# Performance work log

Measured on AMD Instinct MI355X. Metric: run time of the kernel, lower is better.

The kernel has to match this reference:

```python
import jax, jax.numpy as jnp
import numpy as np

NUM_HEADS = 8
ROPE_BASE = 10000.0


def _rope_cache(T, D, dtype=jnp.float32):
    # LLaMA-style rope cache: cos/sin of shape [T, D]
    inv_freq = 1.0 / (ROPE_BASE ** (jnp.arange(0, D, 2, dtype=dtype) / D))
    t = jnp.arange(T, dtype=dtype)
    freqs = t[:, None] * inv_freq[None, :]            # [T, D/2]
    emb = jnp.concatenate([freqs, freqs], axis=-1)    # [T, D]
    return jnp.cos(emb), jnp.sin(emb)


def _rotate_half(x):
    x1, x2 = jnp.split(x, 2, axis=-1)
    return jnp.concatenate([-x2, x1], axis=-1)


def setup_inputs() -> dict:
    key = jax.random.key(0)
    k1, k2, k3 = jax.random.split(key, 3)
    B, T, C = 4, 2048, 512
    x = jax.random.normal(k1, (B, T, C), dtype=jnp.float32)
    Wqkv = jax.random.normal(k2, (C, 3 * C), dtype=jnp.float32) * (1.0 / np.sqrt(C))
    Wproj = jax.random.normal(k3, (C, C), dtype=jnp.float32) * (1.0 / np.sqrt(C))
    return {"x": x, "Wqkv": Wqkv, "Wproj": Wproj}


def reference(x, Wqkv, Wproj):
    B, T, C = x.shape
    H = NUM_HEADS
    D = C // H

    qkv = jnp.einsum('btc,cf->btf', x, Wqkv)          # [B,T,3C]
    qkv = qkv.reshape(B, T, H, 3 * D)
    q, k, v = jnp.split(qkv, 3, axis=-1)              # each [B,T,H,D]
    q = q.transpose(0, 2, 1, 3)                       # [B,H,T,D]
    k = k.transpose(0, 2, 1, 3)
    v = v.transpose(0, 2, 1, 3)

    cos, sin = _rope_cache(T, D, dtype=x.dtype)       # [T,D]
    cos = cos[None, None, :, :]
    sin = sin[None, None, :, :]
    q = q * cos + _rotate_half(q) * sin
    k = k * cos + _rotate_half(k) * sin

    scale = 1.0 / np.sqrt(D)
    scores = jnp.einsum('bhqd,bhkd->bhqk', q, k) * scale  # [B,H,T,T]
    causal = jnp.tril(jnp.ones((T, T), dtype=bool))
    scores = jnp.where(causal[None, None, :, :], scores, jnp.finfo(scores.dtype).min)
    attn = jax.nn.softmax(scores, axis=-1)
    out = jnp.einsum('bhqk,bhkd->bhqd', attn, v)      # [B,H,T,D]
    out = out.transpose(0, 2, 1, 3).reshape(B, T, C)
    return jnp.einsum('btc,cd->btd', out, Wproj)
```

## Files before the change

kernel.cpp:

```cpp
#include <hip/hip_runtime.h>
#include <hip/hip_bf16.h>
#include <stdint.h>

constexpr int Bn = 4;
constexpr int Tn = 2048;
constexpr int Cn = 512;
constexpr int Hn = 8;
constexpr int Dn = 64;
constexpr int BT = Bn * Tn;
constexpr int NQKV = 3 * Cn;

typedef __attribute__((ext_vector_type(4))) float  f32x4;
typedef __attribute__((ext_vector_type(8))) short  s16x8;
typedef __attribute__((ext_vector_type(4))) short  s16x4;

__device__ __forceinline__ short f2bs(float f) {
    __hip_bfloat16 h = __float2bfloat16(f);
    return *reinterpret_cast<short*>(&h);
}

__device__ __forceinline__ void gload16(const short* g, short* l) {
    __builtin_amdgcn_global_load_lds(
        (const __attribute__((address_space(1))) void*)g,
        (__attribute__((address_space(3))) void*)l, 16, 0, 0);
}

__device__ const uint32_t UT[48] = {
    (31u<<16)|(0u<<8)|16u, (31u<<16)|(16u<<8)|32u, (30u<<16)|(15u<<8)|31u, (15u<<16)|(0u<<8)|16u,
    (30u<<16)|(0u<<8)|15u, (29u<<16)|(0u<<8)|15u, (29u<<16)|(15u<<8)|30u, (28u<<16)|(14u<<8)|29u, (14u<<16)|(0u<<8)|15u,
    (28u<<16)|(0u<<8)|14u, (27u<<16)|(0u<<8)|14u, (27u<<16)|(14u<<8)|28u, (26u<<16)|(13u<<8)|27u, (13u<<16)|(0u<<8)|14u,
    (26u<<16)|(0u<<8)|13u, (25u<<16)|(0u<<8)|13u, (25u<<16)|(13u<<8)|26u, (24u<<16)|(12u<<8)|25u, (12u<<16)|(0u<<8)|13u,
    (24u<<16)|(0u<<8)|12u, (23u<<16)|(0u<<8)|12u, (23u<<16)|(12u<<8)|24u, (22u<<16)|(11u<<8)|23u, (11u<<16)|(0u<<8)|12u,
    (22u<<16)|(0u<<8)|11u, (21u<<16)|(0u<<8)|11u, (21u<<16)|(11u<<8)|22u, (20u<<16)|(10u<<8)|21u, (10u<<16)|(0u<<8)|11u,
    (20u<<16)|(0u<<8)|10u, (19u<<16)|(0u<<8)|10u, (19u<<16)|(10u<<8)|20u, (18u<<16)|(9u<<8)|19u,  (9u<<16)|(0u<<8)|10u,
    (18u<<16)|(0u<<8)|9u,  (17u<<16)|(0u<<8)|9u,  (17u<<16)|(9u<<8)|18u,  (16u<<16)|(8u<<8)|17u,  (8u<<16)|(0u<<8)|9u,
    (16u<<16)|(0u<<8)|8u,  (7u<<16)|(0u<<8)|8u,
    (6u<<16)|(0u<<8)|7u, (5u<<16)|(0u<<8)|6u, (4u<<16)|(0u<<8)|5u, (3u<<16)|(0u<<8)|4u,
    (2u<<16)|(0u<<8)|3u, (1u<<16)|(0u<<8)|2u, (0u<<16)|(0u<<8)|1u
};


__global__ __launch_bounds__(256) void k_conv_x(const float* __restrict__ x,
                                                short* __restrict__ xb) {
    int i = blockIdx.x * 256 + threadIdx.x;
    f32x4 v = reinterpret_cast<const f32x4*>(x)[i];
    s16x4 o;
    o[0] = f2bs(v[0]); o[1] = f2bs(v[1]); o[2] = f2bs(v[2]); o[3] = f2bs(v[3]);
    reinterpret_cast<s16x4*>(xb)[i] = o;
}

__global__ __launch_bounds__(256) void k_wTt(const float* __restrict__ Wqkv,
                                             const float* __restrict__ Wproj,
                                             short* __restrict__ wqkvT,
                                             short* __restrict__ wprojT) {
    int bid = blockIdx.x;
    const float* W; short* out; int N, n0, k0;
    if (bid < 192) {
        W = Wqkv; out = wqkvT; N = NQKV;
        n0 = (bid >> 3) * 64; k0 = (bid & 7) * 64;
    } else {
        bid -= 192;
        W = Wproj; out = wprojT; N = Cn;
        n0 = (bid >> 3) * 64; k0 = (bid & 7) * 64;
    }
    __shared__ float lds[64 * 65];
    const int tid = threadIdx.x;
#pragma unroll
    for (int i = 0; i < 16; ++i) {
        int flat = i * 256 + tid;
        int k = flat >> 6, n = flat & 63;
        lds[n * 65 + k] = W[(size_t)(k0 + k) * N + n0 + n];
    }
    __syncthreads();
#pragma unroll
    for (int i = 0; i < 16; ++i) {
        int flat = i * 256 + tid;
        int n = flat >> 6, k = flat & 63;
        out[(size_t)(n0 + n) * 512 + k0 + k] = f2bs(lds[n * 65 + k]);
    }
}

__global__ __launch_bounds__(256) void k_rope(float2* __restrict__ csT) {
    int i = blockIdx.x * 256 + threadIdx.x;
    int t = i >> 6, d = i & 63;
    float inv = exp2f(-(float)(d & 31) * 0.41524101186f);
    float fr = (float)t * inv;
    csT[i] = make_float2(cosf(fr), sinf(fr));
}


template <int MODE>
__global__ __launch_bounds__(256, 2) void gemm_kernel(
    const short* __restrict__ A, const short* __restrict__ Bt,
    const float2* __restrict__ csT,
    short* __restrict__ Qb, short* __restrict__ Kb, short* __restrict__ Vt,
    float* __restrict__ outF) {
    const int m0 = blockIdx.y * 128;
    const int n0 = blockIdx.x * 128;
    const int tid = threadIdx.x;
    const int w = tid >> 6, lane = tid & 63;
    const int qi = lane & 15, g = lane >> 4;
    const int wr = w >> 1, wc = w & 1;

    __shared__ short As[2][128 * 64];
    __shared__ short Bs[2][128 * 64];

    f32x4 acc[4][4];
#pragma unroll
    for (int mt = 0; mt < 4; ++mt)
#pragma unroll
        for (int nt = 0; nt < 4; ++nt) acc[mt][nt] = (f32x4){0.f, 0.f, 0.f, 0.f};

    const int lr = lane >> 3;
    const int lc = (lane & 7) ^ lr;

#define STAGEG(buf, k0)                                                         \
    {                                                                           \
        _Pragma("unroll")                                                       \
        for (int s4_ = 0; s4_ < 4; ++s4_) {                                     \
            int slot_ = s4_ * 4 + w;                                            \
            int r_ = slot_ * 8 + lr;                                            \
            gload16(&A[(size_t)(m0 + r_) * 512 + (k0) + lc * 8],                \
                    &As[buf][slot_ * 512 + lane * 8]);                          \
            gload16(&Bt[(size_t)(n0 + r_) * 512 + (k0) + lc * 8],               \
                    &Bs[buf][slot_ * 512 + lane * 8]);                          \
        }                                                                       \
    }

    STAGEG(0, 0);
    __syncthreads();

    for (int it = 0; it < 8; ++it) {
        if (it + 1 < 8) STAGEG((it + 1) & 1, (it + 1) * 64);
        const int cur = it & 1;
#pragma unroll
        for (int kk = 0; kk < 2; ++kk) {
            s16x8 af[4], bf[4];
#pragma unroll
            for (int mt = 0; mt < 4; ++mt) {
                int row = wr * 64 + mt * 16 + qi;
                af[mt] = *(const s16x8*)&As[cur][row * 64 + (((kk << 2) | g) ^ (qi & 7)) * 8];
            }
#pragma unroll
            for (int nt = 0; nt < 4; ++nt) {
                int row = wc * 64 + nt * 16 + qi;
                bf[nt] = *(const s16x8*)&Bs[cur][row * 64 + (((kk << 2) | g) ^ (qi & 7)) * 8];
            }
#pragma unroll
            for (int mt = 0; mt < 4; ++mt)
#pragma unroll
                for (int nt = 0; nt < 4; ++nt)
                    acc[mt][nt] = __builtin_amdgcn_mfma_f32_16x16x32_bf16(
                        af[mt], bf[nt], acc[mt][nt], 0, 0, 0);
        }
        __syncthreads();
    }
#undef STAGEG

    if (MODE == 1) {
#pragma unroll
        for (int mt = 0; mt < 4; ++mt)
#pragma unroll
            for (int nt = 0; nt < 4; ++nt)
#pragma unroll
                for (int r = 0; r < 4; ++r)
                    outF[(size_t)(m0 + wr * 64 + mt * 16 + 4 * g + r) * 512 +
                         n0 + wc * 64 + nt * 16 + qi] = acc[mt][nt][r];
    } else {
        const int seg64 = (n0 >> 6) + wc;
        const int h = seg64 / 3;
        const int seg = seg64 % 3;
        const int b = m0 >> 11;
        const int tb = (m0 & 2047) + wr * 64;
        const float QSC = 0.125f * 1.44269504f;
        if (seg == 2) {
            const size_t vbase = (size_t)(b * Hn + h) * Dn;
#pragma unroll
            for (int mt = 0; mt < 4; ++mt)
#pragma unroll
                for (int nt = 0; nt < 4; ++nt)
#pragma unroll
                    for (int r = 0; r < 4; ++r) {
                        int t = tb + mt * 16 + 4 * g + r;
                        int d = nt * 16 + qi;
                        int o = t & 31;
                        int jj = (t & ~31) + ((o >> 2) & 3) * 8 + (o >> 4) * 4 + (o & 3);
                        Vt[(vbase + d) * Tn + jj] = f2bs(acc[mt][nt][r]);
                    }
        } else {
            short* dst = (seg == 0) ? Qb : Kb;
            const float post = (seg == 0) ? QSC : 1.0f;
            const size_t headbase = (size_t)(b * Hn + h) * Tn;
#pragma unroll
            for (int mt = 0; mt < 4; ++mt)
#pragma unroll
                for (int nt = 0; nt < 4; ++nt)
#pragma unroll
                    for (int r = 0; r < 4; ++r) {
                        int t = tb + mt * 16 + 4 * g + r;
                        int d = nt * 16 + qi;
                        float val = acc[mt][nt][r];
                        float pv = (nt < 2) ? -acc[mt][nt + 2][r] : acc[mt][nt - 2][r];
                        float2 cs = csT[t * 64 + d];
                        dst[(headbase + t) * Dn + d] = f2bs((val * cs.x + pv * cs.y) * post);
                    }
        }
    }
}


__global__ __launch_bounds__(256, 4) void attn_kernel(const short* __restrict__ Qb,
                                                      const short* __restrict__ Kb,
                                                      const short* __restrict__ Vt,
                                                      short* __restrict__ AO,
                                                      float* __restrict__ Opart,
                                                      float* __restrict__ Lpart) {
    const int idx = blockIdx.x;
    const int bh = idx & 31;
    const uint32_t e = UT[idx >> 5];
    const int qt = e >> 16;
    const int chlo = (e >> 8) & 255, chhi = e & 255;
    const int q0 = qt * 64;
    const int tid = threadIdx.x;
    const int w = tid >> 6, lane = tid & 63;
    const int qi = lane & 15, g = lane >> 4;
    const int b = bh >> 3, h = bh & 7;

    __shared__ short Ks[2][64 * 64];
    __shared__ short Vs[2][64 * 64];

    const short* Qh = Qb + (size_t)bh * Tn * Dn;
    const short* Kh = Kb + (size_t)bh * Tn * Dn;
    const short* Vh = Vt + (size_t)bh * Dn * Tn;

    const int wrow0 = q0 + w * 16;
    s16x8 qf[2];
#pragma unroll
    for (int dh = 0; dh < 2; ++dh)
        qf[dh] = *(const s16x8*)&Qh[(size_t)(wrow0 + qi) * Dn + dh * 32 + g * 8];

    f32x4 O[4];
#pragma unroll
    for (int dt = 0; dt < 4; ++dt) O[dt] = (f32x4){0.f, 0.f, 0.f, 0.f};
    float lsum = 0.f;

    const f32x4 z4 = {0.f, 0.f, 0.f, 0.f};

    const int lr = lane >> 3;
    const int lc = (lane & 7) ^ lr;

#define STAGE(buf, ch)                                                          \
    {                                                                           \
        const int kv0_ = (ch) * 64;                                             \
        _Pragma("unroll")                                                       \
        for (int i_ = 0; i_ < 2; ++i_) {                                        \
            int slot_ = i_ * 4 + w;                                             \
            int r_ = slot_ * 8 + lr;                                            \
            gload16(&Kh[(size_t)(kv0_ + r_) * 64 + lc * 8],                     \
                    &Ks[buf][slot_ * 512 + lane * 8]);                          \
            gload16(&Vh[(size_t)r_ * Tn + kv0_ + lc * 8],                       \
                    &Vs[buf][slot_ * 512 + lane * 8]);                          \
        }                                                                       \
    }

    STAGE(0, chlo);
    __syncthreads();

    for (int ch = chlo; ch < chhi; ++ch) {
        const int rel = ch - chlo;
        if (ch + 1 < chhi) STAGE((rel + 1) & 1, ch + 1);
        const int kv0 = ch * 64;
        const int cur = rel & 1;

        if (kv0 <= wrow0 + 15) {
            f32x4 sacc[4];
#pragma unroll
            for (int sub = 0; sub < 4; ++sub) {
                const int krow = sub * 16 + qi;
                s16x8 ka = *(const s16x8*)&Ks[cur][krow * 64 + ((g ^ (qi & 7))) * 8];
                s16x8 kc = *(const s16x8*)&Ks[cur][krow * 64 + (((4 | g) ^ (qi & 7))) * 8];
                f32x4 t0 = __builtin_amdgcn_mfma_f32_16x16x32_bf16(ka, qf[0], z4, 0, 0, 0);
                sacc[sub] = __builtin_amdgcn_mfma_f32_16x16x32_bf16(kc, qf[1], t0, 0, 0, 0);
            }

            float pe[16];
            if (kv0 + 63 <= wrow0) {
#pragma unroll
                for (int e2 = 0; e2 < 16; ++e2)
                    pe[e2] = exp2f(sacc[e2 >> 2][e2 & 3]);
            } else {
                const int qrow = wrow0 + qi;
#pragma unroll
                for (int sub = 0; sub < 4; ++sub)
#pragma unroll
                    for (int r = 0; r < 4; ++r) {
                        int key = kv0 + sub * 16 + 4 * g + r;
                        pe[sub * 4 + r] = (key <= qrow) ? exp2f(sacc[sub][r]) : 0.f;
                    }
            }
            {
                float a0 = (pe[0] + pe[1]) + (pe[2] + pe[3]);
                float a1 = (pe[4] + pe[5]) + (pe[6] + pe[7]);
                float a2 = (pe[8] + pe[9]) + (pe[10] + pe[11]);
                float a3 = (pe[12] + pe[13]) + (pe[14] + pe[15]);
                lsum += (a0 + a1) + (a2 + a3);
            }
            s16x8 pf[2];
#pragma unroll
            for (int c = 0; c < 2; ++c)
#pragma unroll
                for (int e2 = 0; e2 < 8; ++e2) pf[c][e2] = f2bs(pe[c * 8 + e2]);

#pragma unroll
            for (int c = 0; c < 2; ++c)
#pragma unroll
                for (int dt = 0; dt < 4; ++dt) {
                    const int vrow = dt * 16 + qi;
                    s16x8 vf = *(const s16x8*)&Vs[cur][vrow * 64 +
                                                       ((((c << 2) | g) ^ (qi & 7))) * 8];
                    O[dt] = __builtin_amdgcn_mfma_f32_16x16x32_bf16(
                        pf[c], vf, O[dt], 0, 0, 0);
                }
        }
        __syncthreads();
    }
#undef STAGE

    lsum += __shfl_xor(lsum, 16);
    lsum += __shfl_xor(lsum, 32);

    if (qt < 16) {
#pragma unroll
        for (int r = 0; r < 4; ++r) {
            float li = __shfl(lsum, 4 * g + r);
            float inv = 1.f / li;
            int t = wrow0 + 4 * g + r;
#pragma unroll
            for (int dt = 0; dt < 4; ++dt)
                AO[((size_t)(b * Tn + t)) * Cn + h * 64 + dt * 16 + qi] =
                    f2bs(O[dt][r] * inv);
        }
    } else {
        const int pu = (bh * 16 + (qt - 16)) * 2 + (chlo ? 1 : 0);
        float* Op = Opart + (size_t)pu * 4096;
        if (g == 0) Lpart[pu * 64 + w * 16 + qi] = lsum;
#pragma unroll
        for (int r = 0; r < 4; ++r) {
            int lrow = w * 16 + 4 * g + r;
#pragma unroll
            for (int dt = 0; dt < 4; ++dt)
                Op[lrow * 64 + dt * 16 + qi] = O[dt][r];
        }
    }
}


__global__ __launch_bounds__(256) void combine_kernel(const float* __restrict__ Opart,
                                                      const float* __restrict__ Lpart,
                                                      short* __restrict__ AO) {
    const int u = blockIdx.x;
    const int bh = u & 31, sqt = u >> 5;
    const int pu = (bh * 16 + sqt) * 2;
    const int row = threadIdx.x >> 2;
    const int d0 = (threadIdx.x & 3) * 16;

    const float* O0 = Opart + (size_t)pu * 4096 + row * 64 + d0;
    const float* O1 = O0 + 4096;
    float l = Lpart[pu * 64 + row] + Lpart[(pu + 1) * 64 + row];
    float inv = 1.f / l;

    const int b = bh >> 3, h = bh & 7;
    const int t = (16 + sqt) * 64 + row;
    short* dst = &AO[((size_t)(b * Tn + t)) * Cn + h * 64 + d0];

    s16x8 ov;
#pragma unroll
    for (int j = 0; j < 8; ++j) ov[j] = f2bs((O0[j] + O1[j]) * inv);
    *(s16x8*)dst = ov;
#pragma unroll
    for (int j = 0; j < 8; ++j) ov[j] = f2bs((O0[8 + j] + O1[8 + j]) * inv);
    *(s16x8*)(dst + 8) = ov;
}


extern "C" void kernel_launch(void* const* d_in, const int* in_sizes, int n_in,
                              void* d_out, int out_size, void* d_ws, size_t ws_size,
                              hipStream_t stream) {
    const float* x = (const float*)d_in[0];
    const float* Wqkv = (const float*)d_in[1];
    const float* Wproj = (const float*)d_in[2];
    float* out = (float*)d_out;

    char* ws = (char*)d_ws;
    size_t o = 0;
    short* xb = (short*)(ws + o);      o += (size_t)BT * Cn * 2;
    short* wqkvT = (short*)(ws + o);   o += (size_t)NQKV * Cn * 2;
    short* wprojT = (short*)(ws + o);  o += (size_t)Cn * Cn * 2;
    short* Qb = (short*)(ws + o);      o += (size_t)Bn * Hn * Tn * Dn * 2;
    short* Kb = (short*)(ws + o);      o += (size_t)Bn * Hn * Tn * Dn * 2;
    short* Vt = (short*)(ws + o);      o += (size_t)Bn * Hn * Tn * Dn * 2;
    float2* csT = (float2*)(ws + o);   o += (size_t)Tn * Dn * 8;
    float* Opart = (float*)(ws + o);   o += (size_t)512 * 2 * 4096 * 4;
    float* Lpart = (float*)(ws + o);   o += (size_t)512 * 2 * 64 * 4;

    k_conv_x<<<BT * Cn / 4 / 256, 256, 0, stream>>>(x, xb);
    k_wTt<<<dim3(256), 256, 0, stream>>>(Wqkv, Wproj, wqkvT, wprojT);
    k_rope<<<Tn * Dn / 256, 256, 0, stream>>>(csT);

    gemm_kernel<0><<<dim3(NQKV / 128, BT / 128), 256, 0, stream>>>(
        xb, wqkvT, csT, Qb, Kb, Vt, nullptr);

    attn_kernel<<<dim3(48 * 32), 256, 0, stream>>>(Qb, Kb, Vt, xb ,
                                                   Opart, Lpart);

    combine_kernel<<<dim3(512), 256, 0, stream>>>(Opart, Lpart, xb );

    gemm_kernel<1><<<dim3(Cn / 128, BT / 128), 256, 0, stream>>>(
        xb , wprojT, csT, nullptr, nullptr, nullptr, out);
}
```

Measured before the change: 95.93 us.

## Merge prep kernels into one launch and fuse split-KV combine via atomic counter

The three preprocessing kernels (x conversion, weight transpose, rope cache) become one launch, with an extra block that zeroes a counter array. The separate combine kernel is removed. For split query tiles, each attention block writes its partial result, fences, and increments an atomic counter. The second block to finish reads the other partial and writes the normalized output. This removes two kernel launches and one pass over the partial buffers, at the cost of a threadfence, an atomic, and a divergent tail in the last attention blocks.

```diff
diff --git a/kernel.cpp b/kernel.cpp
--- a/kernel.cpp
+++ b/kernel.cpp
@@ -40,52 +40,58 @@
 };
 
 
-__global__ __launch_bounds__(256) void k_conv_x(const float* __restrict__ x,
-                                                short* __restrict__ xb) {
-    int i = blockIdx.x * 256 + threadIdx.x;
-    f32x4 v = reinterpret_cast<const f32x4*>(x)[i];
-    s16x4 o;
-    o[0] = f2bs(v[0]); o[1] = f2bs(v[1]); o[2] = f2bs(v[2]); o[3] = f2bs(v[3]);
-    reinterpret_cast<s16x4*>(xb)[i] = o;
-}
-
-__global__ __launch_bounds__(256) void k_wTt(const float* __restrict__ Wqkv,
-                                             const float* __restrict__ Wproj,
-                                             short* __restrict__ wqkvT,
-                                             short* __restrict__ wprojT) {
-    int bid = blockIdx.x;
-    const float* W; short* out; int N, n0, k0;
-    if (bid < 192) {
-        W = Wqkv; out = wqkvT; N = NQKV;
-        n0 = (bid >> 3) * 64; k0 = (bid & 7) * 64;
+__global__ __launch_bounds__(256) void k_prep(const float* __restrict__ x,
+                                              const float* __restrict__ Wqkv,
+                                              const float* __restrict__ Wproj,
+                                              short* __restrict__ xb,
+                                              short* __restrict__ wqkvT,
+                                              short* __restrict__ wprojT,
+                                              float2* __restrict__ csT,
+                                              int* __restrict__ cnt) {
+    const int bid = blockIdx.x;
+    const int tid = threadIdx.x;
+    __shared__ float lds[64 * 65];
+
+    if (bid < 4096) {
+        int i = bid * 256 + tid;
+        f32x4 v = reinterpret_cast<const f32x4*>(x)[i];
+        s16x4 o;
+        o[0] = f2bs(v[0]); o[1] = f2bs(v[1]); o[2] = f2bs(v[2]); o[3] = f2bs(v[3]);
+        reinterpret_cast<s16x4*>(xb)[i] = o;
+    } else if (bid < 4352) {
+        int wb = bid - 4096;
+        const float* W; short* out; int N, n0, k0;
+        if (wb < 192) {
+            W = Wqkv; out = wqkvT; N = NQKV;
+            n0 = (wb >> 3) * 64; k0 = (wb & 7) * 64;
+        } else {
+            wb -= 192;
+            W = Wproj; out = wprojT; N = Cn;
+            n0 = (wb >> 3) * 64; k0 = (wb & 7) * 64;
+        }
+#pragma unroll
+        for (int i = 0; i < 16; ++i) {
+            int flat = i * 256 + tid;
+            int k = flat >> 6, n = flat & 63;
+            lds[n * 65 + k] = W[(size_t)(k0 + k) * N + n0 + n];
+        }
+        __syncthreads();
+#pragma unroll
+        for (int i = 0; i < 16; ++i) {
+            int flat = i * 256 + tid;
+            int n = flat >> 6, k = flat & 63;
+            out[(size_t)(n0 + n) * 512 + k0 + k] = f2bs(lds[n * 65 + k]);
+        }
+    } else if (bid < 4864) {
+        int i = (bid - 4352) * 256 + tid;
+        int t = i >> 6, d = i & 63;
+        float inv = exp2f(-(float)(d & 31) * 0.41524101186f);
+        float fr = (float)t * inv;
+        csT[i] = make_float2(cosf(fr), sinf(fr));
     } else {
-        bid -= 192;
-        W = Wproj; out = wprojT; N = Cn;
-        n0 = (bid >> 3) * 64; k0 = (bid & 7) * 64;
-    }
-    __shared__ float lds[64 * 65];
-    const int tid = threadIdx.x;
-#pragma unroll
-    for (int i = 0; i < 16; ++i) {
-        int flat = i * 256 + tid;
-        int k = flat >> 6, n = flat & 63;
-        lds[n * 65 + k] = W[(size_t)(k0 + k) * N + n0 + n];
-    }
-    __syncthreads();
-#pragma unroll
-    for (int i = 0; i < 16; ++i) {
-        int flat = i * 256 + tid;
-        int n = flat >> 6, k = flat & 63;
-        out[(size_t)(n0 + n) * 512 + k0 + k] = f2bs(lds[n * 65 + k]);
-    }
-}
-
-__global__ __launch_bounds__(256) void k_rope(float2* __restrict__ csT) {
-    int i = blockIdx.x * 256 + threadIdx.x;
-    int t = i >> 6, d = i & 63;
-    float inv = exp2f(-(float)(d & 31) * 0.41524101186f);
-    float fr = (float)t * inv;
-    csT[i] = make_float2(cosf(fr), sinf(fr));
+        cnt[tid] = 0;
+        cnt[tid + 256] = 0;
+    }
 }
 
 
@@ -214,7 +220,8 @@
                                                       const short* __restrict__ Vt,
                                                       short* __restrict__ AO,
                                                       float* __restrict__ Opart,
-                                                      float* __restrict__ Lpart) {
+                                                      float* __restrict__ Lpart,
+                                                      int* __restrict__ cnt) {
     const int idx = blockIdx.x;
     const int bh = idx & 31;
     const uint32_t e = UT[idx >> 5];
@@ -228,6 +235,7 @@
 
     __shared__ short Ks[2][64 * 64];
     __shared__ short Vs[2][64 * 64];
+    __shared__ int sflag;
 
     const short* Qh = Qb + (size_t)bh * Tn * Dn;
     const short* Kh = Kb + (size_t)bh * Tn * Dn;
@@ -341,7 +349,9 @@
                     f2bs(O[dt][r] * inv);
         }
     } else {
-        const int pu = (bh * 16 + (qt - 16)) * 2 + (chlo ? 1 : 0);
+        const int sq = qt - 16;
+        const int half = (chlo != 0) ? 1 : 0;
+        const int pu = (bh * 16 + sq) * 2 + half;
         float* Op = Opart + (size_t)pu * 4096;
         if (g == 0) Lpart[pu * 64 + w * 16 + qi] = lsum;
 #pragma unroll
@@ -351,35 +361,27 @@
             for (int dt = 0; dt < 4; ++dt)
                 Op[lrow * 64 + dt * 16 + qi] = O[dt][r];
         }
-    }
-}
-
-
-__global__ __launch_bounds__(256) void combine_kernel(const float* __restrict__ Opart,
-                                                      const float* __restrict__ Lpart,
-                                                      short* __restrict__ AO) {
-    const int u = blockIdx.x;
-    const int bh = u & 31, sqt = u >> 5;
-    const int pu = (bh * 16 + sqt) * 2;
-    const int row = threadIdx.x >> 2;
-    const int d0 = (threadIdx.x & 3) * 16;
-
-    const float* O0 = Opart + (size_t)pu * 4096 + row * 64 + d0;
-    const float* O1 = O0 + 4096;
-    float l = Lpart[pu * 64 + row] + Lpart[(pu + 1) * 64 + row];
-    float inv = 1.f / l;
-
-    const int b = bh >> 3, h = bh & 7;
-    const int t = (16 + sqt) * 64 + row;
-    short* dst = &AO[((size_t)(b * Tn + t)) * Cn + h * 64 + d0];
-
-    s16x8 ov;
-#pragma unroll
-    for (int j = 0; j < 8; ++j) ov[j] = f2bs((O0[j] + O1[j]) * inv);
-    *(s16x8*)dst = ov;
-#pragma unroll
-    for (int j = 0; j < 8; ++j) ov[j] = f2bs((O0[8 + j] + O1[8 + j]) * inv);
-    *(s16x8*)(dst + 8) = ov;
+        __threadfence();
+        if (tid == 0) sflag = atomicAdd(&cnt[bh * 16 + sq], 1);
+        __syncthreads();
+        if (sflag == 1) {
+            __threadfence();
+            const int opu = (bh * 16 + sq) * 2 + (half ^ 1);
+            const float* Oo = Opart + (size_t)opu * 4096;
+            const float* Lo = Lpart + (size_t)opu * 64;
+#pragma unroll
+            for (int r = 0; r < 4; ++r) {
+                int lrow = w * 16 + 4 * g + r;
+                float li = __shfl(lsum, 4 * g + r) + Lo[lrow];
+                float inv = 1.f / li;
+                int t = q0 + lrow;
+#pragma unroll
+                for (int dt = 0; dt < 4; ++dt)
+                    AO[((size_t)(b * Tn + t)) * Cn + h * 64 + dt * 16 + qi] =
+                        f2bs((O[dt][r] + Oo[lrow * 64 + dt * 16 + qi]) * inv);
+            }
+        }
+    }
 }
 
 
@@ -402,18 +404,16 @@
     float2* csT = (float2*)(ws + o);   o += (size_t)Tn * Dn * 8;
     float* Opart = (float*)(ws + o);   o += (size_t)512 * 2 * 4096 * 4;
     float* Lpart = (float*)(ws + o);   o += (size_t)512 * 2 * 64 * 4;
-
-    k_conv_x<<<BT * Cn / 4 / 256, 256, 0, stream>>>(x, xb);
-    k_wTt<<<dim3(256), 256, 0, stream>>>(Wqkv, Wproj, wqkvT, wprojT);
-    k_rope<<<Tn * Dn / 256, 256, 0, stream>>>(csT);
+    int* cnt = (int*)(ws + o);         o += 512 * 4;
+
+    k_prep<<<dim3(4865), 256, 0, stream>>>(x, Wqkv, Wproj, xb, wqkvT, wprojT,
+                                           csT, cnt);
 
     gemm_kernel<0><<<dim3(NQKV / 128, BT / 128), 256, 0, stream>>>(
         xb, wqkvT, csT, Qb, Kb, Vt, nullptr);
 
     attn_kernel<<<dim3(48 * 32), 256, 0, stream>>>(Qb, Kb, Vt, xb ,
-                                                   Opart, Lpart);
-
-    combine_kernel<<<dim3(512), 256, 0, stream>>>(Opart, Lpart, xb );
+                                                   Opart, Lpart, cnt);
 
     gemm_kernel<1><<<dim3(Cn / 128, BT / 128), 256, 0, stream>>>(
         xb , wprojT, csT, nullptr, nullptr, nullptr, out);
```

Measured after the change: 274.1 us. 2.86x slower.
